# Kernel optimization log

Hardware: AMD Instinct MI355X
Metric: run time of the kernel (lower is better)

## Reference

```python
import jax, jax.numpy as jnp
import numpy as np

B = 8192
NV = 778   # MANO vertices
NJ = 16    # LBS joints
PARENTS = np.array([0, 0, 1, 2, 0, 4, 5, 0, 7, 8, 0, 10, 11, 0, 13, 14])


def quat2mat(quat):
    # quat: [N,4] (w,x,y,z) -> [N,3,3]
    q = quat / jnp.linalg.norm(quat, axis=1, keepdims=True)
    w, x, y, z = q[:, 0], q[:, 1], q[:, 2], q[:, 3]
    w2, x2, y2, z2 = w * w, x * x, y * y, z * z
    wx, wy, wz = w * x, w * y, w * z
    xy, xz, yz = x * y, x * z, y * z
    R = jnp.stack([
        w2 + x2 - y2 - z2, 2 * xy - 2 * wz, 2 * wy + 2 * xz,
        2 * wz + 2 * xy, w2 - x2 + y2 - z2, 2 * yz - 2 * wx,
        2 * xz - 2 * wy, 2 * wx + 2 * yz, w2 - x2 - y2 + z2,
    ], axis=1)
    return R.reshape(-1, 3, 3)


def batch_rodrigues(theta):
    # theta: [N,3] axis-angle -> [N,3,3]
    angle = jnp.linalg.norm(theta + 1e-8, axis=1, keepdims=True)
    normalized = theta / angle
    half = angle * 0.5
    quat = jnp.concatenate([jnp.cos(half), jnp.sin(half) * normalized], axis=1)
    return quat2mat(quat)


def qmul(q, r):
    # Hamilton product, (w,x,y,z); q,r: [N,4]
    w1, x1, y1, z1 = q[:, 0], q[:, 1], q[:, 2], q[:, 3]
    w2, x2, y2, z2 = r[:, 0], r[:, 1], r[:, 2], r[:, 3]
    return jnp.stack([
        w1 * w2 - x1 * x2 - y1 * y2 - z1 * z2,
        w1 * x2 + x1 * w2 + y1 * z2 - z1 * y2,
        w1 * y2 - x1 * z2 + y1 * w2 + z1 * x2,
        w1 * z2 + x1 * y2 - y1 * x2 + z1 * w2,
    ], axis=1)


def make_A(R, t):
    # R: [B,J,3,3], t: [B,J,3] -> [B,J,4,4]
    Bn, J = R.shape[0], R.shape[1]
    top = jnp.concatenate([R, t[..., None]], axis=-1)              # [B,J,3,4]
    bot = jnp.broadcast_to(jnp.array([0., 0., 0., 1.], R.dtype), (Bn, J, 1, 4))
    return jnp.concatenate([top, bot], axis=-2)


def mano_forward(theta, delta_quat, user_shape, init_quat, init_trans,
                 v_template, shapedirs, J_regressor, posedirs, weights):
    Bn = theta.shape[0]
    beta = jnp.broadcast_to(user_shape, (Bn, user_shape.shape[-1]))
    v_shaped = (beta @ shapedirs).reshape(Bn, NV, 3) + v_template   # [B,778,3]
    J = jnp.einsum('bvc,vj->bjc', v_shaped, J_regressor)            # [B,21,3]

    Rs = batch_rodrigues(theta.reshape(-1, 3)).reshape(Bn, 15, 3, 3)
    pose_feature = (Rs - jnp.eye(3, dtype=Rs.dtype)).reshape(Bn, 135)
    v_posed = (pose_feature @ posedirs).reshape(Bn, NV, 3) + v_shaped

    quat = qmul(delta_quat, jnp.broadcast_to(init_quat, (Bn, 4)))
    root_R = quat2mat(quat)                                          # [B,3,3]
    Rs_all = jnp.concatenate([root_R[:, None], Rs], axis=1)          # [B,16,3,3]

    Jk = J[:, :NJ]                                                   # [B,16,3]
    rel = Jk - Jk[:, PARENTS]
    rel = rel.at[:, 0].set(Jk[:, 0])                                 # root keeps absolute pos
    A_local = make_A(Rs_all, rel)                                    # [B,16,4,4]

    # kinematic chain (fixed 16-joint tree)
    results = [A_local[:, 0]]
    for i in range(1, NJ):
        results.append(results[PARENTS[i]] @ A_local[:, i])
    G = jnp.stack(results, axis=1)                                   # [B,16,4,4]

    Jw0 = jnp.concatenate([Jk, jnp.zeros((Bn, NJ, 1), Jk.dtype)], axis=-1)
    init_bone = jnp.einsum('bjkl,bjl->bjk', G, Jw0)                  # [B,16,4]
    A = jnp.concatenate([G[..., :3], G[..., 3:] - init_bone[..., None]], axis=-1)

    T = jnp.einsum('vj,bjkl->bvkl', weights, A)                      # [B,778,4,4]
    vp_homo = jnp.concatenate([v_posed, jnp.ones((Bn, NV, 1), v_posed.dtype)], axis=-1)
    verts = jnp.einsum('bvkl,bvl->bvk', T, vp_homo)[..., :3]         # [B,778,3]

    joints = jnp.einsum('bvc,vj->bjc', verts, J_regressor)           # [B,21,3]
    trans = init_trans.reshape(Bn, 1, 3)
    return joints + trans  # get_skin=False path


def setup_inputs() -> dict:
    key = jax.random.key(0)
    ks = jax.random.split(key, 10)
    return {
        'theta': jax.random.normal(ks[0], (B, 45), jnp.float32) * 0.3,
        'delta_quat': jax.random.normal(ks[1], (B, 4), jnp.float32),
        'user_shape': jax.random.normal(ks[2], (1, 10), jnp.float32),
        'init_quat': jax.random.normal(ks[3], (1, 4), jnp.float32),
        'init_trans': jax.random.normal(ks[4], (B, 3), jnp.float32),
        'v_template': jax.random.normal(ks[5], (NV, 3), jnp.float32),
        'shapedirs': jax.random.normal(ks[6], (10, NV * 3), jnp.float32) * 0.01,
        'J_regressor': jax.random.uniform(ks[7], (NV, 21), jnp.float32) / NV,
        'posedirs': jax.random.normal(ks[8], (135, NV * 3), jnp.float32) * 0.01,
        'weights': jax.random.uniform(ks[9], (NV, NJ), jnp.float32),
    }


def reference(theta, delta_quat, user_shape, init_quat, init_trans,
              v_template, shapedirs, J_regressor, posedirs, weights):
    return mano_forward(theta, delta_quat, user_shape, init_quat, init_trans,
                        v_template, shapedirs, J_regressor, posedirs, weights)
```

## Files before the change

kernel.cpp:

```cpp
#include <hip/hip_runtime.h>
#include <math.h>

#define B_SIZE 8192
#define NVERT 778
#define NP 135
#define NEC 416
#define KSPLIT 4

#define OFF_JK    0
#define OFF_C1    64
#define OFF_C0    400
#define OFF_P2    1408
#define OFF_PFT   137488
#define OFF_PPART 1243408
#define OFF_AT    1243408
#define WS_END    2816272

__device__ inline void quat2mat_dev(float qw, float qx, float qy, float qz, float* R) {
  float n = sqrtf(qw*qw + qx*qx + qy*qy + qz*qz);
  float w = qw/n, x = qx/n, y = qy/n, z = qz/n;
  float w2=w*w, x2=x*x, y2=y*y, z2=z*z;
  float wx=w*x, wy=w*y, wz=w*z, xy=x*y, xz=x*z, yz=y*z;
  R[0]=w2+x2-y2-z2; R[1]=2.f*xy-2.f*wz; R[2]=2.f*wy+2.f*xz;
  R[3]=2.f*wz+2.f*xy; R[4]=w2-x2+y2-z2; R[5]=2.f*yz-2.f*wx;
  R[6]=2.f*xz-2.f*wy; R[7]=2.f*wx+2.f*yz; R[8]=w2-x2-y2+z2;
}

__device__ inline void rodrigues_dev(float tx, float ty, float tz, float* R) {
  float ax = tx + 1e-8f, ay = ty + 1e-8f, az = tz + 1e-8f;
  float angle = sqrtf(ax*ax + ay*ay + az*az);
  float nx = tx/angle, ny = ty/angle, nz = tz/angle;
  float half = 0.5f*angle;
  float cw = cosf(half), sw = sinf(half);
  quat2mat_dev(cw, sw*nx, sw*ny, sw*nz, R);
}

__global__ __launch_bounds__(192) void kA(const float* __restrict__ J_regressor,
                                          const float* __restrict__ weights,
                                          const float* __restrict__ posedirs,
                                          const float* __restrict__ user_shape,
                                          const float* __restrict__ v_template,
                                          const float* __restrict__ shapedirs,
                                          float* __restrict__ ws) {
  int tid = threadIdx.x;
  int bid = blockIdx.x;
  __shared__ float ush[10];
  if (tid < 10) ush[tid] = user_shape[tid];

  if (bid >= 104) {
    int j = bid - 104;
    __shared__ float red[3*192];
    float p0 = 0.f, p1 = 0.f, p2 = 0.f;
    __syncthreads();
    for (int v = tid; v < NVERT; v += 192) {
      float jr = J_regressor[v*21 + j];
      #pragma unroll
      for (int c = 0; c < 3; ++c) {
        int e = 3*v + c;
        float t = v_template[e];
        #pragma unroll
        for (int s = 0; s < 10; ++s) t += ush[s]*shapedirs[s*2334 + e];
        float val = jr * t;
        if (c == 0) p0 += val; else if (c == 1) p1 += val; else p2 += val;
      }
    }
    red[0*192+tid] = p0; red[1*192+tid] = p1; red[2*192+tid] = p2;
    __syncthreads();
    if (tid < 3) {
      float s = 0.f;
      for (int t = 0; t < 192; ++t) s += red[tid*192 + t];
      ws[OFF_JK + j*3 + tid] = s;
    }
    return;
  }

  __shared__ float sJR[64*21];
  __shared__ float sW [64*16];
  __shared__ float sB [64*16];
  int ng = bid % 26;
  int ks = bid / 26;
  int vbeg = ks*195;
  int vend = min(NVERT, vbeg + 195);

  int cg = (tid < 84) ? 0 : 1;
  int r4 = (tid < 84) ? tid : tid - 84;
  bool act = (tid < 168);
  int q2 = 4*r4;
  int j2 = q2 >> 4;
  int jb = q2 & 15;

  float acc[4][8];
  #pragma unroll
  for (int r = 0; r < 4; ++r)
    #pragma unroll
    for (int s = 0; s < 8; ++s) acc[r][s] = 0.f;

  for (int v0 = vbeg; v0 < vend; v0 += 64) {
    int kt = min(64, vend - v0);
    __syncthreads();
    for (int idx = tid; idx < kt*21; idx += 192) sJR[idx] = J_regressor[v0*21 + idx];
    for (int idx = tid; idx < kt*16; idx += 192) sW[idx]  = weights[v0*16 + idx];
    for (int idx = tid; idx < 16*64; idx += 192) {
      int s = idx >> 6, iv = idx & 63;
      if (iv < kt) {
        int ec = ng*16 + s;
        float val;
        if (ec > 408) val = 0.f;
        else if (ec == 408) val = 1.f;
        else {
          int c = ec / 136, pp = ec - c*136;
          int e = 3*(v0+iv) + c;
          if (pp == 135) {
            float t = v_template[e];
            #pragma unroll
            for (int s0 = 0; s0 < 10; ++s0) t += ush[s0]*shapedirs[s0*2334 + e];
            val = t;
          } else {
            val = posedirs[pp*2334 + e];
          }
        }
        sB[iv*16 + s] = val;
      }
    }
    __syncthreads();
    if (act) {
      for (int i = 0; i < kt; ++i) {
        float jr = sJR[i*21 + j2];
        float4 w4 = *(const float4*)&sW[i*16 + jb];
        float4 b0 = *(const float4*)&sB[i*16 + cg*8];
        float4 b1 = *(const float4*)&sB[i*16 + cg*8 + 4];
        float wv[4] = {w4.x, w4.y, w4.z, w4.w};
        #pragma unroll
        for (int r = 0; r < 4; ++r) {
          float s2 = jr * wv[r];
          acc[r][0] += s2*b0.x; acc[r][1] += s2*b0.y;
          acc[r][2] += s2*b0.z; acc[r][3] += s2*b0.w;
          acc[r][4] += s2*b1.x; acc[r][5] += s2*b1.y;
          acc[r][6] += s2*b1.z; acc[r][7] += s2*b1.w;
        }
      }
    }
  }
  if (act) {
    float* Pp = ws + OFF_PPART + (size_t)ks*NEC*336;
    #pragma unroll
    for (int s = 0; s < 8; ++s) {
      int ec = ng*16 + cg*8 + s;
      float4 v4 = make_float4(acc[0][s], acc[1][s], acc[2][s], acc[3][s]);
      *(float4*)&Pp[ec*336 + q2] = v4;
    }
  }
}

__global__ void kR(float* __restrict__ ws) {
  int idx = blockIdx.x*256 + threadIdx.x;
  int ec = idx / 336, q2 = idx - ec*336;
  const float* Pp = ws + OFF_PPART;
  float s = 0.f;
  #pragma unroll
  for (int ks = 0; ks < KSPLIT; ++ks) s += Pp[(size_t)ks*NEC*336 + ec*336 + q2];
  int jj2 = q2 >> 4, jj = q2 & 15;
  if (ec < 408) {
    int c = ec / 136, pp = ec - c*136;
    if (pp < 135) ws[OFF_P2 + (size_t)(jj2*135 + pp)*48 + jj*3 + c] = s;
    else          ws[OFF_C0 + jj2*48 + jj*3 + c] = s;
  } else if (ec == 408) {
    ws[OFF_C1 + jj2*16 + jj] = s;
  }
}

__global__ __launch_bounds__(256) void k4_pose(const float* __restrict__ theta,
                                               const float* __restrict__ delta_quat,
                                               const float* __restrict__ init_quat,
                                               float* __restrict__ ws) {
  int b = blockIdx.x*256 + threadIdx.x;
  __shared__ float jk[48], rel[48];
  if (threadIdx.x < 48) {
    float v = ws[OFF_JK + threadIdx.x];
    jk[threadIdx.x] = v;
    int j = threadIdx.x/3, c = threadIdx.x - j*3;
    float r;
    if (j == 0) r = v;
    else {
      int par = (((j-1) % 3) == 0) ? 0 : (j-1);
      r = v - ws[OFF_JK + par*3 + c];
    }
    rel[threadIdx.x] = r;
  }
  __syncthreads();
  float* pfT = ws + OFF_PFT;
  float* AT  = ws + OFF_AT;

  float w1=delta_quat[b*4+0], x1=delta_quat[b*4+1], y1=delta_quat[b*4+2], z1=delta_quat[b*4+3];
  float w2=init_quat[0], x2=init_quat[1], y2=init_quat[2], z2=init_quat[3];
  float qw = w1*w2 - x1*x2 - y1*y2 - z1*z2;
  float qx = w1*x2 + x1*w2 + y1*z2 - z1*y2;
  float qy = w1*y2 - x1*z2 + y1*w2 + z1*x2;
  float qz = w1*z2 + x1*y2 - y1*x2 + z1*w2;
  float Gr[12];
  quat2mat_dev(qw, qx, qy, qz, Gr);
  Gr[9] = rel[0]; Gr[10] = rel[1]; Gr[11] = rel[2];
  #pragma unroll
  for (int c = 0; c < 3; ++c) {
    float g0 = Gr[c*3+0], g1 = Gr[c*3+1], g2 = Gr[c*3+2];
    AT[(size_t)(c*4+0)*B_SIZE + b] = g0;
    AT[(size_t)(c*4+1)*B_SIZE + b] = g1;
    AT[(size_t)(c*4+2)*B_SIZE + b] = g2;
    AT[(size_t)(c*4+3)*B_SIZE + b] = Gr[9+c] - (g0*jk[0] + g1*jk[1] + g2*jk[2]);
  }
  for (int u = 0; u < 5; ++u) {
    float G[12];
    #pragma unroll
    for (int k = 0; k < 12; ++k) G[k] = Gr[k];
    for (int mstep = 0; mstep < 3; ++mstep) {
      int j = 3*u + 1 + mstep;
      int i = j - 1;
      float R[9];
      rodrigues_dev(theta[b*45+3*i+0], theta[b*45+3*i+1], theta[b*45+3*i+2], R);
      pfT[(size_t)(9*i+0)*B_SIZE + b] = R[0]-1.f;
      pfT[(size_t)(9*i+1)*B_SIZE + b] = R[1];
      pfT[(size_t)(9*i+2)*B_SIZE + b] = R[2];
      pfT[(size_t)(9*i+3)*B_SIZE + b] = R[3];
      pfT[(size_t)(9*i+4)*B_SIZE + b] = R[4]-1.f;
      pfT[(size_t)(9*i+5)*B_SIZE + b] = R[5];
      pfT[(size_t)(9*i+6)*B_SIZE + b] = R[6];
      pfT[(size_t)(9*i+7)*B_SIZE + b] = R[7];
      pfT[(size_t)(9*i+8)*B_SIZE + b] = R[8]-1.f;
      float nG[12];
      const float* rj = rel + j*3;
      #pragma unroll
      for (int r3 = 0; r3 < 3; ++r3) {
        float a0 = G[r3*3+0], a1 = G[r3*3+1], a2 = G[r3*3+2];
        nG[r3*3+0] = a0*R[0] + a1*R[3] + a2*R[6];
        nG[r3*3+1] = a0*R[1] + a1*R[4] + a2*R[7];
        nG[r3*3+2] = a0*R[2] + a1*R[5] + a2*R[8];
        nG[9+r3]   = G[9+r3] + a0*rj[0] + a1*rj[1] + a2*rj[2];
      }
      #pragma unroll
      for (int k = 0; k < 12; ++k) G[k] = nG[k];
      const float* jkj = jk + j*3;
      #pragma unroll
      for (int c = 0; c < 3; ++c) {
        float g0 = G[c*3+0], g1 = G[c*3+1], g2 = G[c*3+2];
        AT[(size_t)(j*12 + c*4+0)*B_SIZE + b] = g0;
        AT[(size_t)(j*12 + c*4+1)*B_SIZE + b] = g1;
        AT[(size_t)(j*12 + c*4+2)*B_SIZE + b] = g2;
        AT[(size_t)(j*12 + c*4+3)*B_SIZE + b] = G[9+c] - (g0*jkj[0] + g1*jkj[1] + g2*jkj[2]);
      }
    }
  }
}

__global__ __launch_bounds__(256) void k5_main(const float* __restrict__ init_trans,
                                               const float* __restrict__ ws,
                                               float* __restrict__ out) {
  int g = blockIdx.x;
  int xcd = g & 7, k = g >> 3;
  int br  = ((k & 3) << 3) | xcd;
  int j2  = k >> 2;
  int b   = br*256 + threadIdx.x;

  float4 acc[12];
  const float4* c04 = (const float4*)(ws + OFF_C0 + j2*48);
  #pragma unroll
  for (int i = 0; i < 12; ++i) acc[i] = c04[i];

  const float* pfT = ws + OFF_PFT;
  const float4* P24 = (const float4*)(ws + OFF_P2);
  #pragma unroll 3
  for (int p = 0; p < NP; ++p) {
    float pf = pfT[(size_t)p*B_SIZE + b];
    const float4* Pr = P24 + (size_t)(j2*135 + p)*12;
    #pragma unroll
    for (int i = 0; i < 12; ++i) {
      float4 pv = Pr[i];
      acc[i].x += pf*pv.x; acc[i].y += pf*pv.y;
      acc[i].z += pf*pv.z; acc[i].w += pf*pv.w;
    }
  }

  float m[48];
  #pragma unroll
  for (int i = 0; i < 12; ++i) {
    m[4*i+0] = acc[i].x; m[4*i+1] = acc[i].y;
    m[4*i+2] = acc[i].z; m[4*i+3] = acc[i].w;
  }

  const float* AT  = ws + OFF_AT;
  const float* c1p = ws + OFF_C1 + j2*16;
  float o0 = 0.f, o1 = 0.f, o2 = 0.f;
  #pragma unroll
  for (int j = 0; j < 16; ++j) {
    float c1 = c1p[j];
    float m0 = m[3*j+0], m1 = m[3*j+1], m2 = m[3*j+2];
    #pragma unroll
    for (int k2 = 0; k2 < 3; ++k2) {
      float a0 = AT[(size_t)(j*12 + k2*4+0)*B_SIZE + b];
      float a1 = AT[(size_t)(j*12 + k2*4+1)*B_SIZE + b];
      float a2 = AT[(size_t)(j*12 + k2*4+2)*B_SIZE + b];
      float a3 = AT[(size_t)(j*12 + k2*4+3)*B_SIZE + b];
      float r = a0*m0 + a1*m1 + a2*m2 + a3*c1;
      if (k2 == 0) o0 += r; else if (k2 == 1) o1 += r; else o2 += r;
    }
  }
  size_t ob = ((size_t)b*21 + j2)*3;
  out[ob+0] = o0 + init_trans[b*3+0];
  out[ob+1] = o1 + init_trans[b*3+1];
  out[ob+2] = o2 + init_trans[b*3+2];
}

extern "C" void kernel_launch(void* const* d_in, const int* in_sizes, int n_in,
                              void* d_out, int out_size, void* d_ws, size_t ws_size,
                              hipStream_t stream) {
  const float* theta       = (const float*)d_in[0];
  const float* delta_quat  = (const float*)d_in[1];
  const float* user_shape  = (const float*)d_in[2];
  const float* init_quat   = (const float*)d_in[3];
  const float* init_trans  = (const float*)d_in[4];
  const float* v_template  = (const float*)d_in[5];
  const float* shapedirs   = (const float*)d_in[6];
  const float* J_regressor = (const float*)d_in[7];
  const float* posedirs    = (const float*)d_in[8];
  const float* weights     = (const float*)d_in[9];
  float* out = (float*)d_out;
  float* ws  = (float*)d_ws;

  kA<<<120, 192, 0, stream>>>(J_regressor, weights, posedirs,
                              user_shape, v_template, shapedirs, ws);
  kR<<<546, 256, 0, stream>>>(ws);
  k4_pose<<<32, 256, 0, stream>>>(theta, delta_quat, init_quat, ws);
  k5_main<<<672, 256, 0, stream>>>(init_trans, ws, out);
}
```

Baseline: 169.6 us.

## Fuse four kernels into one cooperative kernel with grid syncs

Replaces the four-launch pipeline with a single cooperative kernel of 672 blocks that uses grid.sync between stages. It raises the weight-precompute K-split from 4 to 16 so more blocks are busy, and stages the per-joint P2/C0/C1 tables in shared memory for the main stage. The aim is to remove launch gaps and the tail effects of the small kernels. The cost is grid-wide barriers, occupancy limited by the large shared array, and a fallback to the old kernels if the cooperative launch fails.

```diff
diff --git a/kernel.cpp b/kernel.cpp
--- a/kernel.cpp
+++ b/kernel.cpp
@@ -1,19 +1,22 @@
 #include <hip/hip_runtime.h>
+#include <hip/hip_cooperative_groups.h>
 #include <math.h>
+
+namespace cg = cooperative_groups;
 
 #define B_SIZE 8192
 #define NVERT 778
 #define NP 135
 #define NEC 416
-#define KSPLIT 4
+#define KS16 16
 
 #define OFF_JK    0
 #define OFF_C1    64
 #define OFF_C0    400
 #define OFF_P2    1408
 #define OFF_PFT   137488
-#define OFF_PPART 1243408
 #define OFF_AT    1243408
+#define OFF_PP    137488
 #define WS_END    2816272
 
 __device__ inline void quat2mat_dev(float qw, float qx, float qy, float qz, float* R) {
@@ -35,18 +38,302 @@
   quat2mat_dev(cw, sw*nx, sw*ny, sw*nz, R);
 }
 
-__global__ __launch_bounds__(192) void kA(const float* __restrict__ J_regressor,
-                                          const float* __restrict__ weights,
-                                          const float* __restrict__ posedirs,
-                                          const float* __restrict__ user_shape,
-                                          const float* __restrict__ v_template,
-                                          const float* __restrict__ shapedirs,
-                                          float* __restrict__ ws) {
+__global__ __launch_bounds__(256, 3)
+void mega(const float* __restrict__ theta,
+          const float* __restrict__ delta_quat,
+          const float* __restrict__ init_quat,
+          const float* __restrict__ init_trans,
+          const float* __restrict__ v_template,
+          const float* __restrict__ user_shape,
+          const float* __restrict__ shapedirs,
+          const float* __restrict__ J_regressor,
+          const float* __restrict__ posedirs,
+          const float* __restrict__ weights,
+          float* __restrict__ ws,
+          float* __restrict__ out) {
+  cg::grid_group grid = cg::this_grid();
+  __shared__ __align__(16) float smem[6656];
+  int tid = threadIdx.x;
+  int bid = blockIdx.x;
+
+  if (bid < 416) {
+    float* sJR = smem;
+    float* sW  = smem + 1344;
+    float* sB  = smem + 2368;
+    float* ush = smem + 3392;
+    if (tid < 10) ush[tid] = user_shape[tid];
+    int ng = bid % 26;
+    int ks = bid / 26;
+    int vbeg = ks*49;
+    int kt = min(NVERT - vbeg, 49);
+    __syncthreads();
+    for (int idx = tid; idx < kt*21; idx += 256) sJR[idx] = J_regressor[vbeg*21 + idx];
+    for (int idx = tid; idx < kt*16; idx += 256) sW[idx]  = weights[vbeg*16 + idx];
+    for (int idx = tid; idx < 16*64; idx += 256) {
+      int s = idx >> 6, iv = idx & 63;
+      if (iv < kt) {
+        int ec = ng*16 + s;
+        float val;
+        if (ec > 408) val = 0.f;
+        else if (ec == 408) val = 1.f;
+        else {
+          int c = ec / 136, pp = ec - c*136;
+          int e = 3*(vbeg+iv) + c;
+          if (pp == 135) {
+            float t = v_template[e];
+            #pragma unroll
+            for (int s0 = 0; s0 < 10; ++s0) t += ush[s0]*shapedirs[s0*2334 + e];
+            val = t;
+          } else {
+            val = posedirs[pp*2334 + e];
+          }
+        }
+        sB[iv*16 + s] = val;
+      }
+    }
+    __syncthreads();
+    if (tid < 168) {
+      int cg2 = (tid < 84) ? 0 : 1;
+      int r4  = (tid < 84) ? tid : tid - 84;
+      int q2 = 4*r4;
+      int j2 = q2 >> 4;
+      int jb = q2 & 15;
+      float acc[4][8];
+      #pragma unroll
+      for (int r = 0; r < 4; ++r)
+        #pragma unroll
+        for (int s = 0; s < 8; ++s) acc[r][s] = 0.f;
+      for (int i = 0; i < kt; ++i) {
+        float jr = sJR[i*21 + j2];
+        float4 w4 = *(const float4*)&sW[i*16 + jb];
+        float4 b0 = *(const float4*)&sB[i*16 + cg2*8];
+        float4 b1 = *(const float4*)&sB[i*16 + cg2*8 + 4];
+        float wv[4] = {w4.x, w4.y, w4.z, w4.w};
+        #pragma unroll
+        for (int r = 0; r < 4; ++r) {
+          float s2 = jr * wv[r];
+          acc[r][0] += s2*b0.x; acc[r][1] += s2*b0.y;
+          acc[r][2] += s2*b0.z; acc[r][3] += s2*b0.w;
+          acc[r][4] += s2*b1.x; acc[r][5] += s2*b1.y;
+          acc[r][6] += s2*b1.z; acc[r][7] += s2*b1.w;
+        }
+      }
+      float* Pp = ws + OFF_PP + (size_t)ks*NEC*336;
+      #pragma unroll
+      for (int s = 0; s < 8; ++s) {
+        int ec = ng*16 + cg2*8 + s;
+        float4 v4 = make_float4(acc[0][s], acc[1][s], acc[2][s], acc[3][s]);
+        *(float4*)&Pp[ec*336 + q2] = v4;
+      }
+    }
+  } else if (bid < 432) {
+    int j = bid - 416;
+    float* red = smem;
+    float* ush = smem + 768;
+    if (tid < 10) ush[tid] = user_shape[tid];
+    __syncthreads();
+    float p0 = 0.f, p1 = 0.f, p2 = 0.f;
+    for (int v = tid; v < NVERT; v += 256) {
+      float jr = J_regressor[v*21 + j];
+      #pragma unroll
+      for (int c = 0; c < 3; ++c) {
+        int e = 3*v + c;
+        float t = v_template[e];
+        #pragma unroll
+        for (int s = 0; s < 10; ++s) t += ush[s]*shapedirs[s*2334 + e];
+        float val = jr * t;
+        if (c == 0) p0 += val; else if (c == 1) p1 += val; else p2 += val;
+      }
+    }
+    red[0*256+tid] = p0; red[1*256+tid] = p1; red[2*256+tid] = p2;
+    __syncthreads();
+    if (tid < 3) {
+      float s = 0.f;
+      for (int t = 0; t < 256; ++t) s += red[tid*256 + t];
+      ws[OFF_JK + j*3 + tid] = s;
+    }
+  }
+  grid.sync();
+
+  if (bid < 546) {
+    int idx = bid*256 + tid;
+    int ec = idx / 336, q2 = idx - ec*336;
+    const float* Pp = ws + OFF_PP;
+    float s = 0.f;
+    #pragma unroll
+    for (int ks = 0; ks < KS16; ++ks) s += Pp[(size_t)ks*NEC*336 + ec*336 + q2];
+    int jj2 = q2 >> 4, jj = q2 & 15;
+    if (ec < 408) {
+      int c = ec / 136, pp = ec - c*136;
+      if (pp < 135) ws[OFF_P2 + (size_t)(jj2*135 + pp)*48 + jj*3 + c] = s;
+      else          ws[OFF_C0 + jj2*48 + jj*3 + c] = s;
+    } else if (ec == 408) {
+      ws[OFF_C1 + jj2*16 + jj] = s;
+    }
+  }
+  grid.sync();
+
+  if (bid < 32) {
+    float* jk  = smem;
+    float* rel = smem + 48;
+    if (tid < 48) {
+      float v = ws[OFF_JK + tid];
+      jk[tid] = v;
+      int j = tid/3, c = tid - j*3;
+      float r;
+      if (j == 0) r = v;
+      else {
+        int par = (((j-1) % 3) == 0) ? 0 : (j-1);
+        r = v - ws[OFF_JK + par*3 + c];
+      }
+      rel[tid] = r;
+    }
+    __syncthreads();
+    int b = bid*256 + tid;
+    float* pfT = ws + OFF_PFT;
+    float* AT  = ws + OFF_AT;
+    float w1=delta_quat[b*4+0], x1=delta_quat[b*4+1], y1=delta_quat[b*4+2], z1=delta_quat[b*4+3];
+    float w2=init_quat[0], x2=init_quat[1], y2=init_quat[2], z2=init_quat[3];
+    float qw = w1*w2 - x1*x2 - y1*y2 - z1*z2;
+    float qx = w1*x2 + x1*w2 + y1*z2 - z1*y2;
+    float qy = w1*y2 - x1*z2 + y1*w2 + z1*x2;
+    float qz = w1*z2 + x1*y2 - y1*x2 + z1*w2;
+    float Gr[12];
+    quat2mat_dev(qw, qx, qy, qz, Gr);
+    Gr[9] = rel[0]; Gr[10] = rel[1]; Gr[11] = rel[2];
+    #pragma unroll
+    for (int c = 0; c < 3; ++c) {
+      float g0 = Gr[c*3+0], g1 = Gr[c*3+1], g2 = Gr[c*3+2];
+      AT[(size_t)(c*4+0)*B_SIZE + b] = g0;
+      AT[(size_t)(c*4+1)*B_SIZE + b] = g1;
+      AT[(size_t)(c*4+2)*B_SIZE + b] = g2;
+      AT[(size_t)(c*4+3)*B_SIZE + b] = Gr[9+c] - (g0*jk[0] + g1*jk[1] + g2*jk[2]);
+    }
+    for (int u = 0; u < 5; ++u) {
+      float G[12];
+      #pragma unroll
+      for (int k = 0; k < 12; ++k) G[k] = Gr[k];
+      for (int mstep = 0; mstep < 3; ++mstep) {
+        int j = 3*u + 1 + mstep;
+        int i = j - 1;
+        float R[9];
+        rodrigues_dev(theta[b*45+3*i+0], theta[b*45+3*i+1], theta[b*45+3*i+2], R);
+        pfT[(size_t)(9*i+0)*B_SIZE + b] = R[0]-1.f;
+        pfT[(size_t)(9*i+1)*B_SIZE + b] = R[1];
+        pfT[(size_t)(9*i+2)*B_SIZE + b] = R[2];
+        pfT[(size_t)(9*i+3)*B_SIZE + b] = R[3];
+        pfT[(size_t)(9*i+4)*B_SIZE + b] = R[4]-1.f;
+        pfT[(size_t)(9*i+5)*B_SIZE + b] = R[5];
+        pfT[(size_t)(9*i+6)*B_SIZE + b] = R[6];
+        pfT[(size_t)(9*i+7)*B_SIZE + b] = R[7];
+        pfT[(size_t)(9*i+8)*B_SIZE + b] = R[8]-1.f;
+        float nG[12];
+        const float* rj = rel + j*3;
+        #pragma unroll
+        for (int r3 = 0; r3 < 3; ++r3) {
+          float a0 = G[r3*3+0], a1 = G[r3*3+1], a2 = G[r3*3+2];
+          nG[r3*3+0] = a0*R[0] + a1*R[3] + a2*R[6];
+          nG[r3*3+1] = a0*R[1] + a1*R[4] + a2*R[7];
+          nG[r3*3+2] = a0*R[2] + a1*R[5] + a2*R[8];
+          nG[9+r3]   = G[9+r3] + a0*rj[0] + a1*rj[1] + a2*rj[2];
+        }
+        #pragma unroll
+        for (int k = 0; k < 12; ++k) G[k] = nG[k];
+        const float* jkj = jk + j*3;
+        #pragma unroll
+        for (int c = 0; c < 3; ++c) {
+          float g0 = G[c*3+0], g1 = G[c*3+1], g2 = G[c*3+2];
+          AT[(size_t)(j*12 + c*4+0)*B_SIZE + b] = g0;
+          AT[(size_t)(j*12 + c*4+1)*B_SIZE + b] = g1;
+          AT[(size_t)(j*12 + c*4+2)*B_SIZE + b] = g2;
+          AT[(size_t)(j*12 + c*4+3)*B_SIZE + b] = G[9+c] - (g0*jkj[0] + g1*jkj[1] + g2*jkj[2]);
+        }
+      }
+    }
+  }
+  grid.sync();
+
+  {
+    int g = bid;
+    int xcd = g & 7, k = g >> 3;
+    int br  = ((k & 3) << 3) | xcd;
+    int j2  = k >> 2;
+    int b   = br*256 + tid;
+
+    float* sP2 = smem;
+    float* sC0 = smem + 6480;
+    float* sC1 = smem + 6528;
+    {
+      float4* d4 = (float4*)sP2;
+      const float4* s4 = (const float4*)(ws + OFF_P2) + (size_t)j2*1620;
+      for (int i = tid; i < 1620; i += 256) d4[i] = s4[i];
+      if (tid < 48) sC0[tid] = ws[OFF_C0 + j2*48 + tid];
+      if (tid < 16) sC1[tid] = ws[OFF_C1 + j2*16 + tid];
+    }
+    __syncthreads();
+
+    float4 acc[12];
+    {
+      const float4* c04 = (const float4*)sC0;
+      #pragma unroll
+      for (int i = 0; i < 12; ++i) acc[i] = c04[i];
+    }
+    const float* pfT = ws + OFF_PFT;
+    const float4* sP24 = (const float4*)sP2;
+    #pragma unroll 3
+    for (int p = 0; p < NP; ++p) {
+      float pf = pfT[(size_t)p*B_SIZE + b];
+      const float4* Pr = sP24 + p*12;
+      #pragma unroll
+      for (int i = 0; i < 12; ++i) {
+        float4 pv = Pr[i];
+        acc[i].x += pf*pv.x; acc[i].y += pf*pv.y;
+        acc[i].z += pf*pv.z; acc[i].w += pf*pv.w;
+      }
+    }
+    float m[48];
+    #pragma unroll
+    for (int i = 0; i < 12; ++i) {
+      m[4*i+0] = acc[i].x; m[4*i+1] = acc[i].y;
+      m[4*i+2] = acc[i].z; m[4*i+3] = acc[i].w;
+    }
+    const float* AT = ws + OFF_AT;
+    float o0 = 0.f, o1 = 0.f, o2 = 0.f;
+    #pragma unroll
+    for (int j = 0; j < 16; ++j) {
+      float c1 = sC1[j];
+      float m0 = m[3*j+0], m1 = m[3*j+1], m2 = m[3*j+2];
+      #pragma unroll
+      for (int k2 = 0; k2 < 3; ++k2) {
+        float a0 = AT[(size_t)(j*12 + k2*4+0)*B_SIZE + b];
+        float a1 = AT[(size_t)(j*12 + k2*4+1)*B_SIZE + b];
+        float a2 = AT[(size_t)(j*12 + k2*4+2)*B_SIZE + b];
+        float a3 = AT[(size_t)(j*12 + k2*4+3)*B_SIZE + b];
+        float r = a0*m0 + a1*m1 + a2*m2 + a3*c1;
+        if (k2 == 0) o0 += r; else if (k2 == 1) o1 += r; else o2 += r;
+      }
+    }
+    size_t ob = ((size_t)b*21 + j2)*3;
+    out[ob+0] = o0 + init_trans[b*3+0];
+    out[ob+1] = o1 + init_trans[b*3+1];
+    out[ob+2] = o2 + init_trans[b*3+2];
+  }
+}
+
+#define KSPLIT_FB 4
+#define OFF_PPART_FB 1243408
+
+__global__ __launch_bounds__(192) void kA_fb(const float* __restrict__ J_regressor,
+                                             const float* __restrict__ weights,
+                                             const float* __restrict__ posedirs,
+                                             const float* __restrict__ user_shape,
+                                             const float* __restrict__ v_template,
+                                             const float* __restrict__ shapedirs,
+                                             float* __restrict__ ws) {
   int tid = threadIdx.x;
   int bid = blockIdx.x;
   __shared__ float ush[10];
   if (tid < 10) ush[tid] = user_shape[tid];
-
   if (bid >= 104) {
     int j = bid - 104;
     __shared__ float red[3*192];
@@ -73,7 +360,6 @@
     }
     return;
   }
-
   __shared__ float sJR[64*21];
   __shared__ float sW [64*16];
   __shared__ float sB [64*16];
@@ -81,20 +367,17 @@
   int ks = bid / 26;
   int vbeg = ks*195;
   int vend = min(NVERT, vbeg + 195);
-
-  int cg = (tid < 84) ? 0 : 1;
+  int cg2 = (tid < 84) ? 0 : 1;
   int r4 = (tid < 84) ? tid : tid - 84;
   bool act = (tid < 168);
   int q2 = 4*r4;
   int j2 = q2 >> 4;
   int jb = q2 & 15;
-
   float acc[4][8];
   #pragma unroll
   for (int r = 0; r < 4; ++r)
     #pragma unroll
     for (int s = 0; s < 8; ++s) acc[r][s] = 0.f;
-
   for (int v0 = vbeg; v0 < vend; v0 += 64) {
     int kt = min(64, vend - v0);
     __syncthreads();
@@ -127,8 +410,8 @@
       for (int i = 0; i < kt; ++i) {
         float jr = sJR[i*21 + j2];
         float4 w4 = *(const float4*)&sW[i*16 + jb];
-        float4 b0 = *(const float4*)&sB[i*16 + cg*8];
-        float4 b1 = *(const float4*)&sB[i*16 + cg*8 + 4];
+        float4 b0 = *(const float4*)&sB[i*16 + cg2*8];
+        float4 b1 = *(const float4*)&sB[i*16 + cg2*8 + 4];
         float wv[4] = {w4.x, w4.y, w4.z, w4.w};
         #pragma unroll
         for (int r = 0; r < 4; ++r) {
@@ -142,23 +425,23 @@
     }
   }
   if (act) {
-    float* Pp = ws + OFF_PPART + (size_t)ks*NEC*336;
+    float* Pp = ws + OFF_PPART_FB + (size_t)ks*NEC*336;
     #pragma unroll
     for (int s = 0; s < 8; ++s) {
-      int ec = ng*16 + cg*8 + s;
+      int ec = ng*16 + cg2*8 + s;
       float4 v4 = make_float4(acc[0][s], acc[1][s], acc[2][s], acc[3][s]);
       *(float4*)&Pp[ec*336 + q2] = v4;
     }
   }
 }
 
-__global__ void kR(float* __restrict__ ws) {
+__global__ void kR_fb(float* __restrict__ ws) {
   int idx = blockIdx.x*256 + threadIdx.x;
   int ec = idx / 336, q2 = idx - ec*336;
-  const float* Pp = ws + OFF_PPART;
+  const float* Pp = ws + OFF_PPART_FB;
   float s = 0.f;
   #pragma unroll
-  for (int ks = 0; ks < KSPLIT; ++ks) s += Pp[(size_t)ks*NEC*336 + ec*336 + q2];
+  for (int ks = 0; ks < KSPLIT_FB; ++ks) s += Pp[(size_t)ks*NEC*336 + ec*336 + q2];
   int jj2 = q2 >> 4, jj = q2 & 15;
   if (ec < 408) {
     int c = ec / 136, pp = ec - c*136;
@@ -169,10 +452,10 @@
   }
 }
 
-__global__ __launch_bounds__(256) void k4_pose(const float* __restrict__ theta,
-                                               const float* __restrict__ delta_quat,
-                                               const float* __restrict__ init_quat,
-                                               float* __restrict__ ws) {
+__global__ __launch_bounds__(256) void k4_fb(const float* __restrict__ theta,
+                                             const float* __restrict__ delta_quat,
+                                             const float* __restrict__ init_quat,
+                                             float* __restrict__ ws) {
   int b = blockIdx.x*256 + threadIdx.x;
   __shared__ float jk[48], rel[48];
   if (threadIdx.x < 48) {
@@ -190,7 +473,6 @@
   __syncthreads();
   float* pfT = ws + OFF_PFT;
   float* AT  = ws + OFF_AT;
-
   float w1=delta_quat[b*4+0], x1=delta_quat[b*4+1], y1=delta_quat[b*4+2], z1=delta_quat[b*4+3];
   float w2=init_quat[0], x2=init_quat[1], y2=init_quat[2], z2=init_quat[3];
   float qw = w1*w2 - x1*x2 - y1*y2 - z1*z2;
@@ -251,20 +533,18 @@
   }
 }
 
-__global__ __launch_bounds__(256) void k5_main(const float* __restrict__ init_trans,
-                                               const float* __restrict__ ws,
-                                               float* __restrict__ out) {
+__global__ __launch_bounds__(256) void k5_fb(const float* __restrict__ init_trans,
+                                             const float* __restrict__ ws,
+                                             float* __restrict__ out) {
   int g = blockIdx.x;
   int xcd = g & 7, k = g >> 3;
   int br  = ((k & 3) << 3) | xcd;
   int j2  = k >> 2;
   int b   = br*256 + threadIdx.x;
-
   float4 acc[12];
   const float4* c04 = (const float4*)(ws + OFF_C0 + j2*48);
   #pragma unroll
   for (int i = 0; i < 12; ++i) acc[i] = c04[i];
-
   const float* pfT = ws + OFF_PFT;
   const float4* P24 = (const float4*)(ws + OFF_P2);
   #pragma unroll 3
@@ -278,14 +558,12 @@
       acc[i].z += pf*pv.z; acc[i].w += pf*pv.w;
     }
   }
-
   float m[48];
   #pragma unroll
   for (int i = 0; i < 12; ++i) {
     m[4*i+0] = acc[i].x; m[4*i+1] = acc[i].y;
     m[4*i+2] = acc[i].z; m[4*i+3] = acc[i].w;
   }
-
   const float* AT  = ws + OFF_AT;
   const float* c1p = ws + OFF_C1 + j2*16;
   float o0 = 0.f, o1 = 0.f, o2 = 0.f;
@@ -325,9 +603,18 @@
   float* out = (float*)d_out;
   float* ws  = (float*)d_ws;
 
-  kA<<<120, 192, 0, stream>>>(J_regressor, weights, posedirs,
-                              user_shape, v_template, shapedirs, ws);
-  kR<<<546, 256, 0, stream>>>(ws);
-  k4_pose<<<32, 256, 0, stream>>>(theta, delta_quat, init_quat, ws);
-  k5_main<<<672, 256, 0, stream>>>(init_trans, ws, out);
-}
+  void* args[] = {
+    (void*)&theta, (void*)&delta_quat, (void*)&init_quat, (void*)&init_trans,
+    (void*)&v_template, (void*)&user_shape, (void*)&shapedirs, (void*)&J_regressor,
+    (void*)&posedirs, (void*)&weights, (void*)&ws, (void*)&out
+  };
+  hipError_t err = hipLaunchCooperativeKernel((void*)mega, dim3(672), dim3(256),
+                                              args, 0, stream);
+  if (err != hipSuccess) {
+    kA_fb<<<120, 192, 0, stream>>>(J_regressor, weights, posedirs,
+                                   user_shape, v_template, shapedirs, ws);
+    kR_fb<<<546, 256, 0, stream>>>(ws);
+    k4_fb<<<32, 256, 0, stream>>>(theta, delta_quat, init_quat, ws);
+    k5_fb<<<672, 256, 0, stream>>>(init_trans, ws, out);
+  }
+}
```

Result: slower. 392.4 us (+131.4%).

## Raise split-K parallelism in precompute and split pose reduction across half-blocks

Applied to the files above, without the earlier changes.

The precompute kernel now splits the vertex reduction into 16 chunks of 49 vertices instead of 4 chunks of 195. That gives 416 GEMM blocks of 256 threads in place of 104, so far more of the GPU is busy. The partial sums are written into the region later reused for pose features, and the reduce kernel sums 16 partials. The joint-regressor blocks now use a tree reduction. The main kernel splits the 135-term pose-blend loop across two half-blocks and combines them through shared memory, doubling the block count; in exchange, half the threads idle during the final skinning step and the reduce kernel reads more partials.

```diff
diff --git a/kernel.cpp b/kernel.cpp
--- a/kernel.cpp
+++ b/kernel.cpp
@@ -5,15 +5,15 @@
 #define NVERT 778
 #define NP 135
 #define NEC 416
-#define KSPLIT 4
+#define KS16 16
 
 #define OFF_JK    0
 #define OFF_C1    64
 #define OFF_C0    400
 #define OFF_P2    1408
 #define OFF_PFT   137488
-#define OFF_PPART 1243408
 #define OFF_AT    1243408
+#define OFF_PP    137488
 #define WS_END    2816272
 
 __device__ inline void quat2mat_dev(float qw, float qx, float qy, float qz, float* R) {
@@ -35,7 +35,7 @@
   quat2mat_dev(cw, sw*nx, sw*ny, sw*nz, R);
 }
 
-__global__ __launch_bounds__(192) void kA(const float* __restrict__ J_regressor,
+__global__ __launch_bounds__(256) void kA(const float* __restrict__ J_regressor,
                                           const float* __restrict__ weights,
                                           const float* __restrict__ posedirs,
                                           const float* __restrict__ user_shape,
@@ -44,15 +44,15 @@
                                           float* __restrict__ ws) {
   int tid = threadIdx.x;
   int bid = blockIdx.x;
-  __shared__ float ush[10];
-  if (tid < 10) ush[tid] = user_shape[tid];
-
-  if (bid >= 104) {
-    int j = bid - 104;
-    __shared__ float red[3*192];
+
+  if (bid >= 416) {
+    int j = bid - 416;
+    __shared__ float red[3*256];
+    __shared__ float ush[10];
+    if (tid < 10) ush[tid] = user_shape[tid];
+    __syncthreads();
     float p0 = 0.f, p1 = 0.f, p2 = 0.f;
-    __syncthreads();
-    for (int v = tid; v < NVERT; v += 192) {
+    for (int v = tid; v < NVERT; v += 256) {
       float jr = J_regressor[v*21 + j];
       #pragma unroll
       for (int c = 0; c < 3; ++c) {
@@ -64,88 +64,85 @@
         if (c == 0) p0 += val; else if (c == 1) p1 += val; else p2 += val;
       }
     }
-    red[0*192+tid] = p0; red[1*192+tid] = p1; red[2*192+tid] = p2;
+    red[0*256+tid] = p0; red[1*256+tid] = p1; red[2*256+tid] = p2;
     __syncthreads();
-    if (tid < 3) {
-      float s = 0.f;
-      for (int t = 0; t < 192; ++t) s += red[tid*192 + t];
-      ws[OFF_JK + j*3 + tid] = s;
-    }
+    for (int s = 128; s > 0; s >>= 1) {
+      if (tid < s) {
+        red[0*256+tid] += red[0*256+tid+s];
+        red[1*256+tid] += red[1*256+tid+s];
+        red[2*256+tid] += red[2*256+tid+s];
+      }
+      __syncthreads();
+    }
+    if (tid < 3) ws[OFF_JK + j*3 + tid] = red[tid*256];
     return;
   }
 
-  __shared__ float sJR[64*21];
-  __shared__ float sW [64*16];
+  __shared__ float sJR[49*21];
+  __shared__ float sW [49*16];
   __shared__ float sB [64*16];
+  __shared__ float ush[10];
+  if (tid < 10) ush[tid] = user_shape[tid];
   int ng = bid % 26;
   int ks = bid / 26;
-  int vbeg = ks*195;
-  int vend = min(NVERT, vbeg + 195);
-
-  int cg = (tid < 84) ? 0 : 1;
-  int r4 = (tid < 84) ? tid : tid - 84;
-  bool act = (tid < 168);
-  int q2 = 4*r4;
-  int j2 = q2 >> 4;
-  int jb = q2 & 15;
-
-  float acc[4][8];
-  #pragma unroll
-  for (int r = 0; r < 4; ++r)
-    #pragma unroll
-    for (int s = 0; s < 8; ++s) acc[r][s] = 0.f;
-
-  for (int v0 = vbeg; v0 < vend; v0 += 64) {
-    int kt = min(64, vend - v0);
-    __syncthreads();
-    for (int idx = tid; idx < kt*21; idx += 192) sJR[idx] = J_regressor[v0*21 + idx];
-    for (int idx = tid; idx < kt*16; idx += 192) sW[idx]  = weights[v0*16 + idx];
-    for (int idx = tid; idx < 16*64; idx += 192) {
-      int s = idx >> 6, iv = idx & 63;
-      if (iv < kt) {
-        int ec = ng*16 + s;
-        float val;
-        if (ec > 408) val = 0.f;
-        else if (ec == 408) val = 1.f;
-        else {
-          int c = ec / 136, pp = ec - c*136;
-          int e = 3*(v0+iv) + c;
-          if (pp == 135) {
-            float t = v_template[e];
-            #pragma unroll
-            for (int s0 = 0; s0 < 10; ++s0) t += ush[s0]*shapedirs[s0*2334 + e];
-            val = t;
-          } else {
-            val = posedirs[pp*2334 + e];
-          }
+  int vbeg = ks*49;
+  int kt = min(NVERT - vbeg, 49);
+  __syncthreads();
+  for (int idx = tid; idx < kt*21; idx += 256) sJR[idx] = J_regressor[vbeg*21 + idx];
+  for (int idx = tid; idx < kt*16; idx += 256) sW[idx]  = weights[vbeg*16 + idx];
+  for (int idx = tid; idx < 16*64; idx += 256) {
+    int s = idx >> 6, iv = idx & 63;
+    if (iv < kt) {
+      int ec = ng*16 + s;
+      float val;
+      if (ec > 408) val = 0.f;
+      else if (ec == 408) val = 1.f;
+      else {
+        int c = ec / 136, pp = ec - c*136;
+        int e = 3*(vbeg+iv) + c;
+        if (pp == 135) {
+          float t = v_template[e];
+          #pragma unroll
+          for (int s0 = 0; s0 < 10; ++s0) t += ush[s0]*shapedirs[s0*2334 + e];
+          val = t;
+        } else {
+          val = posedirs[pp*2334 + e];
         }
-        sB[iv*16 + s] = val;
-      }
-    }
-    __syncthreads();
-    if (act) {
-      for (int i = 0; i < kt; ++i) {
-        float jr = sJR[i*21 + j2];
-        float4 w4 = *(const float4*)&sW[i*16 + jb];
-        float4 b0 = *(const float4*)&sB[i*16 + cg*8];
-        float4 b1 = *(const float4*)&sB[i*16 + cg*8 + 4];
-        float wv[4] = {w4.x, w4.y, w4.z, w4.w};
-        #pragma unroll
-        for (int r = 0; r < 4; ++r) {
-          float s2 = jr * wv[r];
-          acc[r][0] += s2*b0.x; acc[r][1] += s2*b0.y;
-          acc[r][2] += s2*b0.z; acc[r][3] += s2*b0.w;
-          acc[r][4] += s2*b1.x; acc[r][5] += s2*b1.y;
-          acc[r][6] += s2*b1.z; acc[r][7] += s2*b1.w;
-        }
-      }
-    }
-  }
-  if (act) {
-    float* Pp = ws + OFF_PPART + (size_t)ks*NEC*336;
+      }
+      sB[iv*16 + s] = val;
+    }
+  }
+  __syncthreads();
+  if (tid < 168) {
+    int cg2 = (tid < 84) ? 0 : 1;
+    int r4  = (tid < 84) ? tid : tid - 84;
+    int q2 = 4*r4;
+    int j2 = q2 >> 4;
+    int jb = q2 & 15;
+    float acc[4][8];
+    #pragma unroll
+    for (int r = 0; r < 4; ++r)
+      #pragma unroll
+      for (int s = 0; s < 8; ++s) acc[r][s] = 0.f;
+    for (int i = 0; i < kt; ++i) {
+      float jr = sJR[i*21 + j2];
+      float4 w4 = *(const float4*)&sW[i*16 + jb];
+      float4 b0 = *(const float4*)&sB[i*16 + cg2*8];
+      float4 b1 = *(const float4*)&sB[i*16 + cg2*8 + 4];
+      float wv[4] = {w4.x, w4.y, w4.z, w4.w};
+      #pragma unroll
+      for (int r = 0; r < 4; ++r) {
+        float s2 = jr * wv[r];
+        acc[r][0] += s2*b0.x; acc[r][1] += s2*b0.y;
+        acc[r][2] += s2*b0.z; acc[r][3] += s2*b0.w;
+        acc[r][4] += s2*b1.x; acc[r][5] += s2*b1.y;
+        acc[r][6] += s2*b1.z; acc[r][7] += s2*b1.w;
+      }
+    }
+    float* Pp = ws + OFF_PP + (size_t)ks*NEC*336;
     #pragma unroll
     for (int s = 0; s < 8; ++s) {
-      int ec = ng*16 + cg*8 + s;
+      int ec = ng*16 + cg2*8 + s;
       float4 v4 = make_float4(acc[0][s], acc[1][s], acc[2][s], acc[3][s]);
       *(float4*)&Pp[ec*336 + q2] = v4;
     }
@@ -155,10 +152,10 @@
 __global__ void kR(float* __restrict__ ws) {
   int idx = blockIdx.x*256 + threadIdx.x;
   int ec = idx / 336, q2 = idx - ec*336;
-  const float* Pp = ws + OFF_PPART;
+  const float* Pp = ws + OFF_PP;
   float s = 0.f;
   #pragma unroll
-  for (int ks = 0; ks < KSPLIT; ++ks) s += Pp[(size_t)ks*NEC*336 + ec*336 + q2];
+  for (int ks = 0; ks < KS16; ++ks) s += Pp[(size_t)ks*NEC*336 + ec*336 + q2];
   int jj2 = q2 >> 4, jj = q2 & 15;
   if (ec < 408) {
     int c = ec / 136, pp = ec - c*136;
@@ -190,7 +187,6 @@
   __syncthreads();
   float* pfT = ws + OFF_PFT;
   float* AT  = ws + OFF_AT;
-
   float w1=delta_quat[b*4+0], x1=delta_quat[b*4+1], y1=delta_quat[b*4+2], z1=delta_quat[b*4+3];
   float w2=init_quat[0], x2=init_quat[1], y2=init_quat[2], z2=init_quat[3];
   float qw = w1*w2 - x1*x2 - y1*y2 - z1*z2;
@@ -254,23 +250,35 @@
 __global__ __launch_bounds__(256) void k5_main(const float* __restrict__ init_trans,
                                                const float* __restrict__ ws,
                                                float* __restrict__ out) {
+  __shared__ __align__(16) float sM[128*52];
   int g = blockIdx.x;
   int xcd = g & 7, k = g >> 3;
-  int br  = ((k & 3) << 3) | xcd;
-  int j2  = k >> 2;
-  int b   = br*256 + threadIdx.x;
+  int br  = ((k & 7) << 3) | xcd;
+  int j2  = k >> 3;
+  int tid = threadIdx.x;
+  int half = tid >> 7;
+  int bl   = tid & 127;
+  int b    = br*128 + bl;
+
+  int pbeg = half ? 68 : 0;
+  int pend = half ? 135 : 68;
 
   float4 acc[12];
-  const float4* c04 = (const float4*)(ws + OFF_C0 + j2*48);
-  #pragma unroll
-  for (int i = 0; i < 12; ++i) acc[i] = c04[i];
+  if (half == 0) {
+    const float4* c04 = (const float4*)(ws + OFF_C0 + j2*48);
+    #pragma unroll
+    for (int i = 0; i < 12; ++i) acc[i] = c04[i];
+  } else {
+    #pragma unroll
+    for (int i = 0; i < 12; ++i) acc[i] = make_float4(0.f, 0.f, 0.f, 0.f);
+  }
 
   const float* pfT = ws + OFF_PFT;
-  const float4* P24 = (const float4*)(ws + OFF_P2);
-  #pragma unroll 3
-  for (int p = 0; p < NP; ++p) {
+  const float4* P24 = (const float4*)(ws + OFF_P2) + (size_t)j2*1620;
+  #pragma unroll 4
+  for (int p = pbeg; p < pend; ++p) {
     float pf = pfT[(size_t)p*B_SIZE + b];
-    const float4* Pr = P24 + (size_t)(j2*135 + p)*12;
+    const float4* Pr = P24 + p*12;
     #pragma unroll
     for (int i = 0; i < 12; ++i) {
       float4 pv = Pr[i];
@@ -279,34 +287,43 @@
     }
   }
 
-  float m[48];
-  #pragma unroll
-  for (int i = 0; i < 12; ++i) {
-    m[4*i+0] = acc[i].x; m[4*i+1] = acc[i].y;
-    m[4*i+2] = acc[i].z; m[4*i+3] = acc[i].w;
-  }
-
-  const float* AT  = ws + OFF_AT;
-  const float* c1p = ws + OFF_C1 + j2*16;
-  float o0 = 0.f, o1 = 0.f, o2 = 0.f;
-  #pragma unroll
-  for (int j = 0; j < 16; ++j) {
-    float c1 = c1p[j];
-    float m0 = m[3*j+0], m1 = m[3*j+1], m2 = m[3*j+2];
-    #pragma unroll
-    for (int k2 = 0; k2 < 3; ++k2) {
-      float a0 = AT[(size_t)(j*12 + k2*4+0)*B_SIZE + b];
-      float a1 = AT[(size_t)(j*12 + k2*4+1)*B_SIZE + b];
-      float a2 = AT[(size_t)(j*12 + k2*4+2)*B_SIZE + b];
-      float a3 = AT[(size_t)(j*12 + k2*4+3)*B_SIZE + b];
-      float r = a0*m0 + a1*m1 + a2*m2 + a3*c1;
-      if (k2 == 0) o0 += r; else if (k2 == 1) o1 += r; else o2 += r;
-    }
-  }
-  size_t ob = ((size_t)b*21 + j2)*3;
-  out[ob+0] = o0 + init_trans[b*3+0];
-  out[ob+1] = o1 + init_trans[b*3+1];
-  out[ob+2] = o2 + init_trans[b*3+2];
+  if (half == 1) {
+    float4* dst = (float4*)(sM + bl*52);
+    #pragma unroll
+    for (int i = 0; i < 12; ++i) dst[i] = acc[i];
+  }
+  __syncthreads();
+  if (half == 0) {
+    const float4* src = (const float4*)(sM + bl*52);
+    float m[48];
+    #pragma unroll
+    for (int i = 0; i < 12; ++i) {
+      float4 o = src[i];
+      m[4*i+0] = acc[i].x + o.x; m[4*i+1] = acc[i].y + o.y;
+      m[4*i+2] = acc[i].z + o.z; m[4*i+3] = acc[i].w + o.w;
+    }
+    const float* AT  = ws + OFF_AT;
+    const float* c1p = ws + OFF_C1 + j2*16;
+    float o0 = 0.f, o1 = 0.f, o2 = 0.f;
+    #pragma unroll
+    for (int j = 0; j < 16; ++j) {
+      float c1 = c1p[j];
+      float m0 = m[3*j+0], m1 = m[3*j+1], m2 = m[3*j+2];
+      #pragma unroll
+      for (int k2 = 0; k2 < 3; ++k2) {
+        float a0 = AT[(size_t)(j*12 + k2*4+0)*B_SIZE + b];
+        float a1 = AT[(size_t)(j*12 + k2*4+1)*B_SIZE + b];
+        float a2 = AT[(size_t)(j*12 + k2*4+2)*B_SIZE + b];
+        float a3 = AT[(size_t)(j*12 + k2*4+3)*B_SIZE + b];
+        float r = a0*m0 + a1*m1 + a2*m2 + a3*c1;
+        if (k2 == 0) o0 += r; else if (k2 == 1) o1 += r; else o2 += r;
+      }
+    }
+    size_t ob = ((size_t)b*21 + j2)*3;
+    out[ob+0] = o0 + init_trans[b*3+0];
+    out[ob+1] = o1 + init_trans[b*3+1];
+    out[ob+2] = o2 + init_trans[b*3+2];
+  }
 }
 
 extern "C" void kernel_launch(void* const* d_in, const int* in_sizes, int n_in,
@@ -325,9 +342,9 @@
   float* out = (float*)d_out;
   float* ws  = (float*)d_ws;
 
-  kA<<<120, 192, 0, stream>>>(J_regressor, weights, posedirs,
+  kA<<<432, 256, 0, stream>>>(J_regressor, weights, posedirs,
                               user_shape, v_template, shapedirs, ws);
   kR<<<546, 256, 0, stream>>>(ws);
   k4_pose<<<32, 256, 0, stream>>>(theta, delta_quat, init_quat, ws);
-  k5_main<<<672, 256, 0, stream>>>(init_trans, ws, out);
-}
+  k5_main<<<1344, 256, 0, stream>>>(init_trans, ws, out);
+}
```

After: 278.7 us. 1.64x slower.
